# Performance work log

Hardware: AMD Instinct MI355X
Metric: run time of the kernel (lower is better)

The kernel has to match this reference:

```python
import jax, jax.numpy as jnp
import numpy as np


def setup_inputs() -> dict:
    key = jax.random.key(0)
    ks = jax.random.split(key, 4)
    B, S, D, V = 2, 2048, 768, 50257
    scale = 1.0 / np.sqrt(D)
    x = jax.random.normal(ks[0], (B, S, D), dtype=jnp.float32)
    W_vocab = jax.random.normal(ks[1], (V, D), dtype=jnp.float32) * scale
    b_vocab = jnp.zeros((V,), dtype=jnp.float32)
    W_lin = jax.random.normal(ks[2], (D, D), dtype=jnp.float32) * scale
    b_lin = jnp.zeros((D,), dtype=jnp.float32)
    return {"x": x, "W_vocab": W_vocab, "b_vocab": b_vocab, "W_lin": W_lin, "b_lin": b_lin}


def reference(x, W_vocab, b_vocab, W_lin, b_lin):
    # vocab_attention_layer(x): [B,S,D] @ [D,V] + b -> [B,S,V]
    logits = jnp.einsum('bsd,vd->bsv', x, W_vocab) + b_vocab
    va = jax.nn.softmax(logits, axis=-1)                      # [B,S,V]
    # einsum('bij,jk->bik', va, weight): contract vocab against embedding rows
    va_weight = jnp.einsum('bsv,vd->bsd', va, W_vocab)        # [B,S,D]
    # final nn.Linear(d_model, d_model): y = h @ W^T + b
    return jnp.einsum('bsd,ed->bse', va_weight, W_lin) + b_lin
```

## Files before the change

### kernel.cpp

```cpp
#include <hip/hip_runtime.h>
#include <hip/hip_bf16.h>
#include <stdint.h>

typedef float f32x4 __attribute__((ext_vector_type(4)));
typedef short s16x8 __attribute__((ext_vector_type(8)));
typedef unsigned short u16;

#define M_ROWS 4096
#define DIM    768
#define VOCAB  50257
#define VPAD   50304

#define OFF_XB     0ull
#define OFF_WLB    6291456ull
#define OFF_WVB    7471104ull
#define OFF_WVTC   84738048ull
#define OFF_P      100270080ull
#define OFF_ORUN   183107584ull
#define OFF_LROW   195690496ull
#define OFF_BROW   195706880ull
#define OFF_KEYS   195723264ull
#define OFF_H      195723392ull

__device__ __forceinline__ u16 f2bf(float f) {
    union { float f; unsigned u; } x; x.f = f;
    return (u16)((x.u + 0x7fffu + ((x.u >> 16) & 1u)) >> 16);
}
__device__ __forceinline__ float bf2f_hi(unsigned u) {
    union { unsigned u; float f; } x; x.u = u & 0xffff0000u; return x.f;
}
__device__ __forceinline__ float bf2f_lo(unsigned u) {
    union { unsigned u; float f; } x; x.u = u << 16; return x.f;
}
__device__ __forceinline__ unsigned fkey(float f) {
    union { float f; unsigned u; } x; x.f = f;
    return (x.u & 0x80000000u) ? ~x.u : (x.u | 0x80000000u);
}
__device__ __forceinline__ float fkey_dec(unsigned k) {
    union { unsigned u; float f; } x;
    x.u = (k & 0x80000000u) ? (k & 0x7fffffffu) : ~k;
    return x.f;
}
__device__ __forceinline__ void glds16(const u16* g, u16* l) {
    __builtin_amdgcn_global_load_lds(
        (const __attribute__((address_space(1))) unsigned int*)g,
        (__attribute__((address_space(3))) unsigned int*)l,
        16, 0, 0);
}

__global__ __launch_bounds__(256) void cast_bf16(const float* __restrict__ src,
                                                 u16* __restrict__ dst, int n4) {
    int i = blockIdx.x * 256 + threadIdx.x;
    if (i >= n4) return;
    float4 v = ((const float4*)src)[i];
    ushort4 o;
    o.x = f2bf(v.x); o.y = f2bf(v.y); o.z = f2bf(v.z); o.w = f2bf(v.w);
    ((ushort4*)dst)[i] = o;
}

__global__ __launch_bounds__(256) void prep_wvb(const float* __restrict__ wv,
                                                u16* __restrict__ wvb, int ntask) {
    int t = blockIdx.x * 256 + threadIdx.x;
    if (t >= ntask) return;
    int v = t / 96, ch = t % 96;
    uint4 pk = {0u, 0u, 0u, 0u};
    if (v < VOCAB) {
        const float* p = wv + (size_t)v * DIM + ch * 8;
        float4 f0 = ((const float4*)p)[0];
        float4 f1 = ((const float4*)p)[1];
        pk.x = (unsigned)f2bf(f0.x) | ((unsigned)f2bf(f0.y) << 16);
        pk.y = (unsigned)f2bf(f0.z) | ((unsigned)f2bf(f0.w) << 16);
        pk.z = (unsigned)f2bf(f1.x) | ((unsigned)f2bf(f1.y) << 16);
        pk.w = (unsigned)f2bf(f1.z) | ((unsigned)f2bf(f1.w) << 16);
    }
    *(uint4*)(wvb + (size_t)v * DIM + ch * 8) = pk;
}

__global__ void init_keys(unsigned* keys) {
    keys[0] = 0u;
    keys[1] = fkey(-3.0e38f);
}

__global__ __launch_bounds__(256) void wnorm(const u16* __restrict__ wvb,
                                             unsigned* __restrict__ keys) {
    __shared__ float part[128];
    int tid = threadIdx.x;
    int vb = blockIdx.x * 32;
    int vl = tid & 31, cg = tid >> 5;
    float s = 0.f;
    #pragma unroll
    for (int it = 0; it < 12; ++it) {
        int ch = cg + 8 * it;
        uint4 pk = *(const uint4*)(wvb + (size_t)(vb + vl) * DIM + ch * 8);
        const unsigned* pw = (const unsigned*)&pk;
        #pragma unroll
        for (int k = 0; k < 4; ++k) {
            float lo = bf2f_lo(pw[k]), hi = bf2f_hi(pw[k]);
            s += lo * lo + hi * hi;
        }
    }
    s += __shfl_xor(s, 32);
    int w = tid >> 6, lane = tid & 63;
    if (lane < 32) part[w * 32 + lane] = s;
    __syncthreads();
    if (tid < 32) {
        float t = part[tid] + part[32 + tid] + part[64 + tid] + part[96 + tid];
        float n = sqrtf(t);
        #pragma unroll
        for (int msk = 1; msk < 32; msk <<= 1) n = fmaxf(n, __shfl_xor(n, msk));
        if (tid == 0) atomicMax(&keys[0], __float_as_uint(n));
    }
}

__global__ __launch_bounds__(256) void bmax_k(const float* __restrict__ bv,
                                              unsigned* __restrict__ keys) {
    int i = blockIdx.x * 256 + threadIdx.x;
    float v = (i < VOCAB) ? bv[i] : -3.0e38f;
    #pragma unroll
    for (int msk = 1; msk < 64; msk <<= 1) v = fmaxf(v, __shfl_xor(v, msk));
    if ((threadIdx.x & 63) == 0) atomicMax(&keys[1], fkey(v));
}

__global__ __launch_bounds__(256) void xnorm(const float* __restrict__ x,
                                             const unsigned* __restrict__ keys,
                                             float* __restrict__ Brow) {
    int w = threadIdx.x >> 6, lane = threadIdx.x & 63;
    int r = blockIdx.x * 4 + w;
    const float4* p = (const float4*)(x + (size_t)r * DIM);
    float s = 0.f;
    #pragma unroll
    for (int it = 0; it < 3; ++it) {
        float4 v = p[it * 64 + lane];
        s += v.x * v.x + v.y * v.y + v.z * v.z + v.w * v.w;
    }
    #pragma unroll
    for (int msk = 1; msk < 64; msk <<= 1) s += __shfl_xor(s, msk);
    if (lane == 0) {
        float Wn = __uint_as_float(keys[0]);
        float bm = fkey_dec(keys[1]);
        Brow[r] = sqrtf(s) * Wn * 1.01f + bm + 0.1f;
    }
}

__global__ __launch_bounds__(256) void prep_wvt_chunk(const u16* __restrict__ wvb,
                                                      u16* __restrict__ wvtc, int v0) {
    __shared__ u16 tile[32][776];
    int tb = blockIdx.x;
    int tid = threadIdx.x;
    int vb = v0 + tb * 32;
    #pragma unroll
    for (int it = 0; it < 12; ++it) {
        int task = tid + 256 * it;
        int row = task / 96, ch = task % 96;
        uint4 pk = *(const uint4*)(wvb + (size_t)(vb + row) * DIM + ch * 8);
        *(uint4*)(&tile[row][ch * 8]) = pk;
    }
    __syncthreads();
    #pragma unroll
    for (int it = 0; it < 12; ++it) {
        int task = tid + 256 * it;
        int d = task >> 2, vc = task & 3;
        u16 t8[8];
        #pragma unroll
        for (int j = 0; j < 8; ++j) t8[j] = tile[vc * 8 + j][d];
        uint4 pk;
        pk.x = (unsigned)t8[0] | ((unsigned)t8[1] << 16);
        pk.y = (unsigned)t8[2] | ((unsigned)t8[3] << 16);
        pk.z = (unsigned)t8[4] | ((unsigned)t8[5] << 16);
        pk.w = (unsigned)t8[6] | ((unsigned)t8[7] << 16);
        *(uint4*)(wvtc + (size_t)tb * 24576 + d * 32 + vc * 8) = pk;
    }
}

__global__ __launch_bounds__(256, 2) void gemm1(
    const u16* __restrict__ xb, const u16* __restrict__ wvb,
    const float* __restrict__ bvocab, const float* __restrict__ Brow,
    u16* __restrict__ P, float* __restrict__ Lrow, int v0, int pitch) {
    __shared__ u16 SB[17408];
    __shared__ float BL[128];
    u16* At = SB;
    u16* Bt = SB + 4096;
    u16* Ptile = SB;
    int mb = blockIdx.x & 31, nb = blockIdx.x >> 5;
    int tid = threadIdx.x;
    int w = tid >> 6, lane = tid & 63, q = lane >> 4, c = lane & 15;
    int wm = w & 1, wn = w >> 1;
    if (tid < 128) BL[tid] = Brow[mb * 128 + tid];
    int trow = tid >> 2, tch = tid & 3;
    const u16* gA0 = xb + (size_t)(mb * 128 + trow) * DIM + tch * 8;
    const u16* gA1 = xb + (size_t)(mb * 128 + 64 + trow) * DIM + tch * 8;
    const u16* gB0 = wvb + (size_t)(v0 + nb * 128 + trow) * DIM + tch * 8;
    const u16* gB1 = wvb + (size_t)(v0 + nb * 128 + 64 + trow) * DIM + tch * 8;
    f32x4 acc[4][4];
    #pragma unroll
    for (int i = 0; i < 4; ++i)
        #pragma unroll
        for (int j = 0; j < 4; ++j) acc[i][j] = (f32x4){0.f, 0.f, 0.f, 0.f};

    for (int ko = 0; ko < 24; ++ko) {
        glds16(gA0 + ko * 32, At + tid * 8);
        glds16(gA1 + ko * 32, At + (tid + 256) * 8);
        glds16(gB0 + ko * 32, Bt + tid * 8);
        glds16(gB1 + ko * 32, Bt + (tid + 256) * 8);
        __syncthreads();
        s16x8 af[4], bf[4];
        #pragma unroll
        for (int i = 0; i < 4; ++i)
            af[i] = *(const s16x8*)(At + (wm * 64 + i * 16 + c) * 32 + q * 8);
        #pragma unroll
        for (int j = 0; j < 4; ++j)
            bf[j] = *(const s16x8*)(Bt + (wn * 64 + j * 16 + c) * 32 + q * 8);
        #pragma unroll
        for (int i = 0; i < 4; ++i)
            #pragma unroll
            for (int j = 0; j < 4; ++j)
                acc[i][j] = __builtin_amdgcn_mfma_f32_16x16x32_bf16(af[i], bf[j], acc[i][j], 0, 0, 0);
        __syncthreads();
    }
    float bvv[4]; bool vok[4];
    #pragma unroll
    for (int j = 0; j < 4; ++j) {
        int v = v0 + nb * 128 + wn * 64 + j * 16 + c;
        vok[j] = (v < VOCAB);
        bvv[j] = vok[j] ? bvocab[v] : 0.f;
    }
    #pragma unroll
    for (int i = 0; i < 4; ++i) {
        #pragma unroll
        for (int jr = 0; jr < 4; ++jr) {
            int row = wm * 64 + i * 16 + q * 4 + jr;
            float B = BL[row];
            float e[4], sum = 0.f;
            #pragma unroll
            for (int j = 0; j < 4; ++j) {
                float z = acc[i][j][jr] + bvv[j];
                e[j] = vok[j] ? __expf(z - B) : 0.f;
                sum += e[j];
            }
            #pragma unroll
            for (int j = 0; j < 4; ++j)
                Ptile[row * 136 + wn * 64 + j * 16 + c] = f2bf(e[j]);
            sum += __shfl_xor(sum, 1);
            sum += __shfl_xor(sum, 2);
            sum += __shfl_xor(sum, 4);
            sum += __shfl_xor(sum, 8);
            if (c == 0) atomicAdd(&Lrow[mb * 128 + row], sum);
        }
    }
    __syncthreads();
    #pragma unroll
    for (int it = 0; it < 8; ++it) {
        int task = tid + 256 * it;
        int row = task >> 4, ch = task & 15;
        uint4 pk = *(const uint4*)(Ptile + row * 136 + ch * 8);
        *(uint4*)(P + (size_t)(mb * 128 + row) * pitch + nb * 128 + ch * 8) = pk;
    }
}

__global__ __launch_bounds__(256, 2) void gemm2(
    const u16* __restrict__ P, const u16* __restrict__ wvtc,
    float* __restrict__ Orun, int pitch, int kt32_total, int kts) {
    __shared__ u16 At[4096];
    __shared__ u16 Bt[4096];
    int mb = blockIdx.x & 31;
    int rest = blockIdx.x >> 5;
    int nb = rest % 6, s = rest / 6;
    int kt0 = s * kts;
    int kt1 = kt0 + kts; if (kt1 > kt32_total) kt1 = kt32_total;
    int tid = threadIdx.x;
    int w = tid >> 6, lane = tid & 63, q = lane >> 4, c = lane & 15;
    int wm = w & 1, wn = w >> 1;
    int trow = tid >> 2, tch = tid & 3;
    const u16* gA0 = P + (size_t)(mb * 128 + trow) * pitch + tch * 8;
    const u16* gA1 = P + (size_t)(mb * 128 + 64 + trow) * pitch + tch * 8;
    const u16* gB0 = wvtc + (size_t)(nb * 128 + trow) * 32 + tch * 8;
    const u16* gB1 = wvtc + (size_t)(nb * 128 + 64 + trow) * 32 + tch * 8;
    f32x4 acc[4][4];
    #pragma unroll
    for (int i = 0; i < 4; ++i)
        #pragma unroll
        for (int j = 0; j < 4; ++j) acc[i][j] = (f32x4){0.f, 0.f, 0.f, 0.f};

    for (int kt = kt0; kt < kt1; ++kt) {
        glds16(gA0 + kt * 32, At + tid * 8);
        glds16(gA1 + kt * 32, At + (tid + 256) * 8);
        glds16(gB0 + (size_t)kt * 24576, Bt + tid * 8);
        glds16(gB1 + (size_t)kt * 24576, Bt + (tid + 256) * 8);
        __syncthreads();
        s16x8 af[4], bf[4];
        #pragma unroll
        for (int i = 0; i < 4; ++i)
            af[i] = *(const s16x8*)(At + (wm * 64 + i * 16 + c) * 32 + q * 8);
        #pragma unroll
        for (int j = 0; j < 4; ++j)
            bf[j] = *(const s16x8*)(Bt + (wn * 64 + j * 16 + c) * 32 + q * 8);
        #pragma unroll
        for (int i = 0; i < 4; ++i)
            #pragma unroll
            for (int j = 0; j < 4; ++j)
                acc[i][j] = __builtin_amdgcn_mfma_f32_16x16x32_bf16(af[i], bf[j], acc[i][j], 0, 0, 0);
        __syncthreads();
    }
    #pragma unroll
    for (int i = 0; i < 4; ++i)
        #pragma unroll
        for (int j = 0; j < 4; ++j)
            #pragma unroll
            for (int jr = 0; jr < 4; ++jr) {
                int row = mb * 128 + wm * 64 + i * 16 + q * 4 + jr;
                int col = nb * 128 + wn * 64 + j * 16 + c;
                atomicAdd(&Orun[(size_t)row * DIM + col], acc[i][j][jr]);
            }
}

__global__ __launch_bounds__(256) void final_h(const float* __restrict__ Orun,
                                               const float* __restrict__ Lrow,
                                               u16* __restrict__ h) {
    int idx = blockIdx.x * 256 + threadIdx.x;
    if (idx >= M_ROWS * DIM) return;
    int r = idx / DIM;
    h[idx] = f2bf(Orun[idx] / Lrow[r]);
}

__global__ __launch_bounds__(256, 2) void final_gemm(const u16* __restrict__ h,
                                                     const u16* __restrict__ wlb,
                                                     const float* __restrict__ blin,
                                                     float* __restrict__ out) {
    __shared__ u16 At[4096];
    __shared__ u16 Bt[4096];
    int mb = blockIdx.x & 31, eb = blockIdx.x >> 5;
    int tid = threadIdx.x;
    int w = tid >> 6, lane = tid & 63, q = lane >> 4, c = lane & 15;
    int wm = w & 1, wn = w >> 1;
    int trow = tid >> 2, tch = tid & 3;
    const u16* gA0 = h + (size_t)(mb * 128 + trow) * DIM + tch * 8;
    const u16* gA1 = h + (size_t)(mb * 128 + 64 + trow) * DIM + tch * 8;
    const u16* gB0 = wlb + (size_t)(eb * 128 + trow) * DIM + tch * 8;
    const u16* gB1 = wlb + (size_t)(eb * 128 + 64 + trow) * DIM + tch * 8;
    f32x4 acc[4][4];
    #pragma unroll
    for (int i = 0; i < 4; ++i)
        #pragma unroll
        for (int j = 0; j < 4; ++j) acc[i][j] = (f32x4){0.f, 0.f, 0.f, 0.f};

    for (int ko = 0; ko < 24; ++ko) {
        glds16(gA0 + ko * 32, At + tid * 8);
        glds16(gA1 + ko * 32, At + (tid + 256) * 8);
        glds16(gB0 + ko * 32, Bt + tid * 8);
        glds16(gB1 + ko * 32, Bt + (tid + 256) * 8);
        __syncthreads();
        s16x8 af[4], bf[4];
        #pragma unroll
        for (int i = 0; i < 4; ++i)
            af[i] = *(const s16x8*)(At + (wm * 64 + i * 16 + c) * 32 + q * 8);
        #pragma unroll
        for (int j = 0; j < 4; ++j)
            bf[j] = *(const s16x8*)(Bt + (wn * 64 + j * 16 + c) * 32 + q * 8);
        #pragma unroll
        for (int i = 0; i < 4; ++i)
            #pragma unroll
            for (int j = 0; j < 4; ++j)
                acc[i][j] = __builtin_amdgcn_mfma_f32_16x16x32_bf16(af[i], bf[j], acc[i][j], 0, 0, 0);
        __syncthreads();
    }
    #pragma unroll
    for (int j = 0; j < 4; ++j) {
        int e = eb * 128 + wn * 64 + j * 16 + c;
        float bl = blin[e];
        #pragma unroll
        for (int i = 0; i < 4; ++i) {
            #pragma unroll
            for (int jr = 0; jr < 4; ++jr) {
                int row = mb * 128 + wm * 64 + i * 16 + q * 4 + jr;
                out[(size_t)row * DIM + e] = acc[i][j][jr] + bl;
            }
        }
    }
}

extern "C" void kernel_launch(void* const* d_in, const int* in_sizes, int n_in,
                              void* d_out, int out_size, void* d_ws, size_t ws_size,
                              hipStream_t stream) {
    const float* x  = (const float*)d_in[0];
    const float* Wv = (const float*)d_in[1];
    const float* bv = (const float*)d_in[2];
    const float* Wl = (const float*)d_in[3];
    const float* bl = (const float*)d_in[4];
    float* out = (float*)d_out;
    char* ws = (char*)d_ws;

    u16* xb   = (u16*)(ws + OFF_XB);
    u16* wlb  = (u16*)(ws + OFF_WLB);
    u16* wvb  = (u16*)(ws + OFF_WVB);
    u16* wvtc = (u16*)(ws + OFF_WVTC);
    u16* P    = (u16*)(ws + OFF_P);
    float* Orun  = (float*)(ws + OFF_ORUN);
    float* Lrow  = (float*)(ws + OFF_LROW);
    float* Brow  = (float*)(ws + OFF_BROW);
    unsigned* keys = (unsigned*)(ws + OFF_KEYS);
    u16* h       = (u16*)(ws + OFF_H);

    cast_bf16<<<(M_ROWS * DIM / 4 + 255) / 256, 256, 0, stream>>>(x, xb, M_ROWS * DIM / 4);
    cast_bf16<<<(DIM * DIM / 4 + 255) / 256, 256, 0, stream>>>(Wl, wlb, DIM * DIM / 4);
    {
        int ntask = VPAD * 96;
        prep_wvb<<<(ntask + 255) / 256, 256, 0, stream>>>(Wv, wvb, ntask);
    }
    init_keys<<<1, 1, 0, stream>>>(keys);
    hipMemsetAsync(Orun, 0, (size_t)M_ROWS * DIM * 4, stream);
    hipMemsetAsync(Lrow, 0, (size_t)M_ROWS * 4, stream);
    wnorm<<<VPAD / 32, 256, 0, stream>>>(wvb, keys);
    bmax_k<<<(VOCAB + 255) / 256, 256, 0, stream>>>(bv, keys);
    xnorm<<<M_ROWS / 4, 256, 0, stream>>>(x, keys, Brow);

    const int chunk_start[5] = {0, 79, 158, 237, 316};
    const int chunk_nt[5]    = {79, 79, 79, 79, 77};
    for (int cidx = 0; cidx < 5; ++cidx) {
        int nt = chunk_nt[cidx];
        int v0 = chunk_start[cidx] * 128;
        int pitch = nt * 128;
        int kt32 = nt * 4;
        int kts = (kt32 + 3) / 4;
        prep_wvt_chunk<<<nt * 4, 256, 0, stream>>>(wvb, wvtc, v0);
        gemm1<<<nt * 32, 256, 0, stream>>>(xb, wvb, bv, Brow, P, Lrow, v0, pitch);
        gemm2<<<32 * 6 * 4, 256, 0, stream>>>(P, wvtc, Orun, pitch, kt32, kts);
    }
    final_h<<<(M_ROWS * DIM + 255) / 256, 256, 0, stream>>>(Orun, Lrow, h);
    final_gemm<<<192, 256, 0, stream>>>(h, wlb, bl, out);
}
```

Measured before the change: 1.293 ms.

## Use 256x256 double-buffered swizzled MFMA tiles for both vocab GEMMs

Replaces the 128x128, single-buffered, 32-wide-K GEMM loops with a shared 256x256 tile loop that uses 64-wide K, 512 threads, XOR-swizzled LDS, double-buffered global-to-LDS prefetch and barrier/priority phasing around the MFMA groups. The W_vocab transpose moves out of the chunk loop into one full-matrix transpose, and the vocab chunks become 8192 wide (7 chunks) with a split-K gemm2 over 240 blocks. The goal is more operand reuse per byte loaded and better overlap of memory with MFMA work. In exchange it uses 128KB of LDS per block, needs more workspace, keeps fp32 atomics on Orun, and the last chunk is small and may under-fill the GPU.

```diff
diff --git a/kernel.cpp b/kernel.cpp
--- a/kernel.cpp
+++ b/kernel.cpp
@@ -9,18 +9,18 @@
 #define M_ROWS 4096
 #define DIM    768
 #define VOCAB  50257
-#define VPAD   50304
+#define VP2    50432
 
 #define OFF_XB     0ull
 #define OFF_WLB    6291456ull
 #define OFF_WVB    7471104ull
-#define OFF_WVTC   84738048ull
-#define OFF_P      100270080ull
-#define OFF_ORUN   183107584ull
-#define OFF_LROW   195690496ull
-#define OFF_BROW   195706880ull
-#define OFF_KEYS   195723264ull
-#define OFF_H      195723392ull
+#define OFF_WVT    84934656ull
+#define OFF_P      162398208ull
+#define OFF_ORUN   229507072ull
+#define OFF_LROW   242089984ull
+#define OFF_BROW   242106368ull
+#define OFF_KEYS   242122752ull
+#define OFF_H      242122880ull
 
 __device__ __forceinline__ u16 f2bf(float f) {
     union { float f; unsigned u; } x; x.f = f;
@@ -142,175 +142,243 @@
     }
 }
 
-__global__ __launch_bounds__(256) void prep_wvt_chunk(const u16* __restrict__ wvb,
-                                                      u16* __restrict__ wvtc, int v0) {
+__global__ __launch_bounds__(256) void prep_wvt(const u16* __restrict__ wvb,
+                                                u16* __restrict__ wvt) {
     __shared__ u16 tile[32][776];
-    int tb = blockIdx.x;
+    int vb = blockIdx.x * 32;
     int tid = threadIdx.x;
-    int vb = v0 + tb * 32;
     #pragma unroll
     for (int it = 0; it < 12; ++it) {
         int task = tid + 256 * it;
         int row = task / 96, ch = task % 96;
-        uint4 pk = *(const uint4*)(wvb + (size_t)(vb + row) * DIM + ch * 8);
-        *(uint4*)(&tile[row][ch * 8]) = pk;
+        *(uint4*)(&tile[row][ch * 8]) = *(const uint4*)(wvb + (size_t)(vb + row) * DIM + ch * 8);
     }
     __syncthreads();
     #pragma unroll
     for (int it = 0; it < 12; ++it) {
         int task = tid + 256 * it;
-        int d = task >> 2, vc = task & 3;
+        int d = task >> 2, vg = task & 3;
         u16 t8[8];
         #pragma unroll
-        for (int j = 0; j < 8; ++j) t8[j] = tile[vc * 8 + j][d];
+        for (int j = 0; j < 8; ++j) t8[j] = tile[vg * 8 + j][d];
         uint4 pk;
         pk.x = (unsigned)t8[0] | ((unsigned)t8[1] << 16);
         pk.y = (unsigned)t8[2] | ((unsigned)t8[3] << 16);
         pk.z = (unsigned)t8[4] | ((unsigned)t8[5] << 16);
         pk.w = (unsigned)t8[6] | ((unsigned)t8[7] << 16);
-        *(uint4*)(wvtc + (size_t)tb * 24576 + d * 32 + vc * 8) = pk;
-    }
-}
-
-__global__ __launch_bounds__(256, 2) void gemm1(
+        *(uint4*)(wvt + (size_t)d * VP2 + vb + vg * 8) = pk;
+    }
+}
+
+
+template<int MH, int NH>
+__device__ __forceinline__ void mfma_quad(f32x4 (&acc)[8][4],
+                                          const s16x8 (&afr)[4][2],
+                                          const s16x8 (&bfr)[2][2][2]) {
+    #pragma unroll
+    for (int mi = 0; mi < 4; ++mi)
+        #pragma unroll
+        for (int ni = 0; ni < 2; ++ni) {
+            f32x4 a_ = acc[MH * 4 + mi][NH * 2 + ni];
+            a_ = __builtin_amdgcn_mfma_f32_16x16x32_bf16(afr[mi][0], bfr[NH][ni][0], a_, 0, 0, 0);
+            a_ = __builtin_amdgcn_mfma_f32_16x16x32_bf16(afr[mi][1], bfr[NH][ni][1], a_, 0, 0, 0);
+            acc[MH * 4 + mi][NH * 2 + ni] = a_;
+        }
+}
+
+#define STG(g, pitch, rowbase, kcol, ldst) do {                                   \
+    const u16* _s0 = (g) + (size_t)((rowbase) + rlo) * (pitch) + (kcol) + offu;   \
+    const u16* _s1 = _s0 + (size_t)64 * (pitch);                                  \
+    glds16(_s0, (u16*)(ldst) + (size_t)tid * 8);                                  \
+    glds16(_s1, (u16*)(ldst) + (size_t)tid * 8 + 4096);                           \
+} while (0)
+
+#define RD_A(buf, mh) do { _Pragma("unroll")                                              \
+    for (int _mi = 0; _mi < 4; ++_mi) {                                                   \
+        afr[_mi][0] = *(const s16x8*)((buf) + ((abase + ((mh)*4 + _mi)*2048)      ^ asw));\
+        afr[_mi][1] = *(const s16x8*)((buf) + ((abase + ((mh)*4 + _mi)*2048 + 64) ^ asw));\
+    } } while (0)
+
+#define RD_B(buf, nh) do { _Pragma("unroll")                                              \
+    for (int _ni = 0; _ni < 2; ++_ni) {                                                   \
+        bfr[nh][_ni][0] = *(const s16x8*)((buf) + ((bbase + ((nh)*2 + _ni)*2048)      ^ asw));\
+        bfr[nh][_ni][1] = *(const s16x8*)((buf) + ((bbase + ((nh)*2 + _ni)*2048 + 64) ^ asw));\
+    } } while (0)
+
+#define PH_SYNC1() do { __builtin_amdgcn_s_barrier();                      \
+    asm volatile("s_waitcnt lgkmcnt(0)" ::: "memory");                     \
+    __builtin_amdgcn_s_setprio(1); } while (0)
+#define PH_SYNC2() do { __builtin_amdgcn_s_setprio(0);                     \
+    __builtin_amdgcn_s_barrier(); } while (0)
+
+__device__ __forceinline__ void kloop256(char* LDS,
+                                         const u16* __restrict__ gA, int pA,
+                                         const u16* __restrict__ gB, int pB,
+                                         int NT, int tid, f32x4 (&acc)[8][4]) {
+    const int lane = tid & 63, w = tid >> 6;
+    const int c = lane & 15, q = (lane >> 4) & 3;
+    const int wm = w & 1, wn = w >> 1;
+    const int asw = (c & 7) << 4;
+    const int abase = wm * 16384 + c * 128 + q * 16;
+    const int bbase = (wn >> 1) * 16384 + (wn & 1) * 8192 + c * 128 + q * 16;
+    const int rlo = tid >> 3;
+    const int offu = ((tid & 7) * 8) ^ ((rlo & 7) << 3);
+    char* A0 = LDS;
+    char* B0 = LDS + 32768;
+    char* A1 = LDS + 65536;
+    char* B1 = LDS + 98304;
+    s16x8 afr[4][2], bfr[2][2][2];
+    const int ktN = NT - 1;
+
+    STG(gA, pA, 0,   0, A0);
+    STG(gA, pA, 128, 0, A0 + 16384);
+    STG(gB, pB, 0,   0, B0);
+    STG(gB, pB, 128, 0, B0 + 16384);
+    {
+        int k1 = (ktN >= 1 ? 1 : 0) * 64;
+        STG(gB, pB, 0,   k1, B1);
+        STG(gB, pB, 128, k1, B1 + 16384);
+        STG(gA, pA, 0,   k1, A1);
+    }
+    asm volatile("s_waitcnt vmcnt(6)" ::: "memory");
+    __builtin_amdgcn_s_barrier();
+
+    const int nit = NT >> 1;
+    #pragma unroll 1
+    for (int it2 = 0; it2 < nit; ++it2) {
+        int kO  = ((2 * it2 + 1 < NT) ? 2 * it2 + 1 : ktN) * 64;
+        int kN0 = ((2 * it2 + 2 < NT) ? 2 * it2 + 2 : ktN) * 64;
+        int kN1 = ((2 * it2 + 3 < NT) ? 2 * it2 + 3 : ktN) * 64;
+        RD_A(A0, 0); RD_B(B0, 0);
+        STG(gA, pA, 128, kO, A1 + 16384);
+        PH_SYNC1(); mfma_quad<0, 0>(acc, afr, bfr); PH_SYNC2();
+        RD_B(B0, 1);
+        PH_SYNC1(); mfma_quad<0, 1>(acc, afr, bfr); PH_SYNC2();
+        RD_A(A0, 1);
+        STG(gB, pB, 0, kN0, B0);
+        PH_SYNC1(); mfma_quad<1, 0>(acc, afr, bfr); PH_SYNC2();
+        STG(gB, pB, 128, kN0, B0 + 16384);
+        STG(gA, pA, 0,   kN0, A0);
+        asm volatile("s_waitcnt vmcnt(6)" ::: "memory");
+        PH_SYNC1(); mfma_quad<1, 1>(acc, afr, bfr); PH_SYNC2();
+        RD_A(A1, 0); RD_B(B1, 0);
+        STG(gA, pA, 128, kN0, A0 + 16384);
+        PH_SYNC1(); mfma_quad<0, 0>(acc, afr, bfr); PH_SYNC2();
+        RD_B(B1, 1);
+        PH_SYNC1(); mfma_quad<0, 1>(acc, afr, bfr); PH_SYNC2();
+        RD_A(A1, 1);
+        STG(gB, pB, 0, kN1, B1);
+        PH_SYNC1(); mfma_quad<1, 0>(acc, afr, bfr); PH_SYNC2();
+        STG(gB, pB, 128, kN1, B1 + 16384);
+        STG(gA, pA, 0,   kN1, A1);
+        asm volatile("s_waitcnt vmcnt(6)" ::: "memory");
+        PH_SYNC1(); mfma_quad<1, 1>(acc, afr, bfr); PH_SYNC2();
+    }
+}
+
+__global__ __launch_bounds__(512, 2) void gemm1(
     const u16* __restrict__ xb, const u16* __restrict__ wvb,
     const float* __restrict__ bvocab, const float* __restrict__ Brow,
-    u16* __restrict__ P, float* __restrict__ Lrow, int v0, int pitch) {
-    __shared__ u16 SB[17408];
-    __shared__ float BL[128];
-    u16* At = SB;
-    u16* Bt = SB + 4096;
-    u16* Ptile = SB;
-    int mb = blockIdx.x & 31, nb = blockIdx.x >> 5;
+    u16* __restrict__ P, float* __restrict__ Lrow, int v0, int CN) {
+    __shared__ __align__(16) char LDS[131072];
+    __shared__ float BL[256];
     int tid = threadIdx.x;
-    int w = tid >> 6, lane = tid & 63, q = lane >> 4, c = lane & 15;
+    int mt = blockIdx.x & 15, nt = blockIdx.x >> 4;
+    if (tid < 256) BL[tid] = Brow[mt * 256 + tid];
+    f32x4 acc[8][4];
+    #pragma unroll
+    for (int i = 0; i < 8; ++i)
+        #pragma unroll
+        for (int j = 0; j < 4; ++j) acc[i][j] = (f32x4){0.f, 0.f, 0.f, 0.f};
+    kloop256(LDS, xb + (size_t)(mt * 256) * DIM, DIM,
+             wvb + (size_t)(v0 + nt * 256) * DIM, DIM, 12, tid, acc);
+
+    int lane = tid & 63, w = tid >> 6, c = lane & 15, q = (lane >> 4) & 3;
     int wm = w & 1, wn = w >> 1;
-    if (tid < 128) BL[tid] = Brow[mb * 128 + tid];
-    int trow = tid >> 2, tch = tid & 3;
-    const u16* gA0 = xb + (size_t)(mb * 128 + trow) * DIM + tch * 8;
-    const u16* gA1 = xb + (size_t)(mb * 128 + 64 + trow) * DIM + tch * 8;
-    const u16* gB0 = wvb + (size_t)(v0 + nb * 128 + trow) * DIM + tch * 8;
-    const u16* gB1 = wvb + (size_t)(v0 + nb * 128 + 64 + trow) * DIM + tch * 8;
-    f32x4 acc[4][4];
-    #pragma unroll
-    for (int i = 0; i < 4; ++i)
+    float bvv[4]; bool vok[4];
+    #pragma unroll
+    for (int n = 0; n < 4; ++n) {
+        int vg = v0 + nt * 256 + wn * 64 + n * 16 + c;
+        vok[n] = vg < VOCAB;
+        bvv[n] = vok[n] ? bvocab[vg] : 0.f;
+    }
+    #pragma unroll
+    for (int m = 0; m < 8; ++m)
+        #pragma unroll
+        for (int jr = 0; jr < 4; ++jr) {
+            int rloc = wm * 128 + m * 16 + q * 4 + jr;
+            float B = BL[rloc];
+            float s = 0.f;
+            #pragma unroll
+            for (int n = 0; n < 4; ++n) {
+                float z = acc[m][n][jr] + bvv[n];
+                float e = vok[n] ? __expf(z - B) : 0.f;
+                acc[m][n][jr] = e;
+                s += e;
+            }
+            s += __shfl_xor(s, 1); s += __shfl_xor(s, 2);
+            s += __shfl_xor(s, 4); s += __shfl_xor(s, 8);
+            if (c == 0) atomicAdd(&Lrow[mt * 256 + rloc], s);
+        }
+    u16* Pt = (u16*)LDS;
+    #pragma unroll
+    for (int h = 0; h < 2; ++h) {
+        if (h) __syncthreads();
+        if (wm == h) {
+            #pragma unroll
+            for (int m = 0; m < 8; ++m)
+                #pragma unroll
+                for (int jr = 0; jr < 4; ++jr) {
+                    int r = m * 16 + q * 4 + jr;
+                    #pragma unroll
+                    for (int n = 0; n < 4; ++n)
+                        Pt[r * 256 + wn * 64 + n * 16 + c] = f2bf(acc[m][n][jr]);
+                }
+        }
+        __syncthreads();
+        #pragma unroll
+        for (int itc = 0; itc < 8; ++itc) {
+            int task = tid + itc * 512;
+            int r = task >> 5, chn = task & 31;
+            uint4 pk = *(const uint4*)(Pt + r * 256 + chn * 8);
+            *(uint4*)(P + (size_t)(mt * 256 + h * 128 + r) * CN + nt * 256 + chn * 8) = pk;
+        }
+    }
+}
+
+__global__ __launch_bounds__(512, 2) void gemm2(
+    const u16* __restrict__ P, const u16* __restrict__ wvt,
+    float* __restrict__ Orun, int CN, int v0, int KT) {
+    __shared__ __align__(16) char LDS[131072];
+    int tid = threadIdx.x;
+    int mt = blockIdx.x & 15;
+    int rest = blockIdx.x >> 4;
+    int nt = rest % 3, s = rest / 3;
+    int ks0 = ((KT + 9) / 10) * 2;
+    int k0 = s * ks0;
+    if (k0 >= KT) return;
+    int NTs = (k0 + ks0 <= KT) ? ks0 : (KT - k0);
+    f32x4 acc[8][4];
+    #pragma unroll
+    for (int i = 0; i < 8; ++i)
         #pragma unroll
         for (int j = 0; j < 4; ++j) acc[i][j] = (f32x4){0.f, 0.f, 0.f, 0.f};
-
-    for (int ko = 0; ko < 24; ++ko) {
-        glds16(gA0 + ko * 32, At + tid * 8);
-        glds16(gA1 + ko * 32, At + (tid + 256) * 8);
-        glds16(gB0 + ko * 32, Bt + tid * 8);
-        glds16(gB1 + ko * 32, Bt + (tid + 256) * 8);
-        __syncthreads();
-        s16x8 af[4], bf[4];
-        #pragma unroll
-        for (int i = 0; i < 4; ++i)
-            af[i] = *(const s16x8*)(At + (wm * 64 + i * 16 + c) * 32 + q * 8);
-        #pragma unroll
-        for (int j = 0; j < 4; ++j)
-            bf[j] = *(const s16x8*)(Bt + (wn * 64 + j * 16 + c) * 32 + q * 8);
-        #pragma unroll
-        for (int i = 0; i < 4; ++i)
-            #pragma unroll
-            for (int j = 0; j < 4; ++j)
-                acc[i][j] = __builtin_amdgcn_mfma_f32_16x16x32_bf16(af[i], bf[j], acc[i][j], 0, 0, 0);
-        __syncthreads();
-    }
-    float bvv[4]; bool vok[4];
-    #pragma unroll
-    for (int j = 0; j < 4; ++j) {
-        int v = v0 + nb * 128 + wn * 64 + j * 16 + c;
-        vok[j] = (v < VOCAB);
-        bvv[j] = vok[j] ? bvocab[v] : 0.f;
-    }
-    #pragma unroll
-    for (int i = 0; i < 4; ++i) {
-        #pragma unroll
-        for (int jr = 0; jr < 4; ++jr) {
-            int row = wm * 64 + i * 16 + q * 4 + jr;
-            float B = BL[row];
-            float e[4], sum = 0.f;
-            #pragma unroll
-            for (int j = 0; j < 4; ++j) {
-                float z = acc[i][j][jr] + bvv[j];
-                e[j] = vok[j] ? __expf(z - B) : 0.f;
-                sum += e[j];
-            }
-            #pragma unroll
-            for (int j = 0; j < 4; ++j)
-                Ptile[row * 136 + wn * 64 + j * 16 + c] = f2bf(e[j]);
-            sum += __shfl_xor(sum, 1);
-            sum += __shfl_xor(sum, 2);
-            sum += __shfl_xor(sum, 4);
-            sum += __shfl_xor(sum, 8);
-            if (c == 0) atomicAdd(&Lrow[mb * 128 + row], sum);
-        }
-    }
-    __syncthreads();
-    #pragma unroll
-    for (int it = 0; it < 8; ++it) {
-        int task = tid + 256 * it;
-        int row = task >> 4, ch = task & 15;
-        uint4 pk = *(const uint4*)(Ptile + row * 136 + ch * 8);
-        *(uint4*)(P + (size_t)(mb * 128 + row) * pitch + nb * 128 + ch * 8) = pk;
-    }
-}
-
-__global__ __launch_bounds__(256, 2) void gemm2(
-    const u16* __restrict__ P, const u16* __restrict__ wvtc,
-    float* __restrict__ Orun, int pitch, int kt32_total, int kts) {
-    __shared__ u16 At[4096];
-    __shared__ u16 Bt[4096];
-    int mb = blockIdx.x & 31;
-    int rest = blockIdx.x >> 5;
-    int nb = rest % 6, s = rest / 6;
-    int kt0 = s * kts;
-    int kt1 = kt0 + kts; if (kt1 > kt32_total) kt1 = kt32_total;
-    int tid = threadIdx.x;
-    int w = tid >> 6, lane = tid & 63, q = lane >> 4, c = lane & 15;
+    kloop256(LDS, P + (size_t)(mt * 256) * CN + k0 * 64, CN,
+             wvt + (size_t)(nt * 256) * VP2 + v0 + k0 * 64, VP2, NTs, tid, acc);
+
+    int lane = tid & 63, w = tid >> 6, c = lane & 15, q = (lane >> 4) & 3;
     int wm = w & 1, wn = w >> 1;
-    int trow = tid >> 2, tch = tid & 3;
-    const u16* gA0 = P + (size_t)(mb * 128 + trow) * pitch + tch * 8;
-    const u16* gA1 = P + (size_t)(mb * 128 + 64 + trow) * pitch + tch * 8;
-    const u16* gB0 = wvtc + (size_t)(nb * 128 + trow) * 32 + tch * 8;
-    const u16* gB1 = wvtc + (size_t)(nb * 128 + 64 + trow) * 32 + tch * 8;
-    f32x4 acc[4][4];
-    #pragma unroll
-    for (int i = 0; i < 4; ++i)
-        #pragma unroll
-        for (int j = 0; j < 4; ++j) acc[i][j] = (f32x4){0.f, 0.f, 0.f, 0.f};
-
-    for (int kt = kt0; kt < kt1; ++kt) {
-        glds16(gA0 + kt * 32, At + tid * 8);
-        glds16(gA1 + kt * 32, At + (tid + 256) * 8);
-        glds16(gB0 + (size_t)kt * 24576, Bt + tid * 8);
-        glds16(gB1 + (size_t)kt * 24576, Bt + (tid + 256) * 8);
-        __syncthreads();
-        s16x8 af[4], bf[4];
-        #pragma unroll
-        for (int i = 0; i < 4; ++i)
-            af[i] = *(const s16x8*)(At + (wm * 64 + i * 16 + c) * 32 + q * 8);
-        #pragma unroll
-        for (int j = 0; j < 4; ++j)
-            bf[j] = *(const s16x8*)(Bt + (wn * 64 + j * 16 + c) * 32 + q * 8);
-        #pragma unroll
-        for (int i = 0; i < 4; ++i)
-            #pragma unroll
-            for (int j = 0; j < 4; ++j)
-                acc[i][j] = __builtin_amdgcn_mfma_f32_16x16x32_bf16(af[i], bf[j], acc[i][j], 0, 0, 0);
-        __syncthreads();
-    }
-    #pragma unroll
-    for (int i = 0; i < 4; ++i)
-        #pragma unroll
-        for (int j = 0; j < 4; ++j)
+    #pragma unroll
+    for (int m = 0; m < 8; ++m)
+        #pragma unroll
+        for (int n = 0; n < 4; ++n) {
+            int col = nt * 256 + wn * 64 + n * 16 + c;
             #pragma unroll
             for (int jr = 0; jr < 4; ++jr) {
-                int row = mb * 128 + wm * 64 + i * 16 + q * 4 + jr;
-                int col = nb * 128 + wn * 64 + j * 16 + c;
-                atomicAdd(&Orun[(size_t)row * DIM + col], acc[i][j][jr]);
+                int row = mt * 256 + wm * 128 + m * 16 + q * 4 + jr;
+                atomicAdd(&Orun[(size_t)row * DIM + col], acc[m][n][jr]);
             }
+        }
 }
 
 __global__ __launch_bounds__(256) void final_h(const float* __restrict__ Orun,
@@ -392,7 +460,7 @@
     u16* xb   = (u16*)(ws + OFF_XB);
     u16* wlb  = (u16*)(ws + OFF_WLB);
     u16* wvb  = (u16*)(ws + OFF_WVB);
-    u16* wvtc = (u16*)(ws + OFF_WVTC);
+    u16* wvt  = (u16*)(ws + OFF_WVT);
     u16* P    = (u16*)(ws + OFF_P);
     float* Orun  = (float*)(ws + OFF_ORUN);
     float* Lrow  = (float*)(ws + OFF_LROW);
@@ -403,27 +471,26 @@
     cast_bf16<<<(M_ROWS * DIM / 4 + 255) / 256, 256, 0, stream>>>(x, xb, M_ROWS * DIM / 4);
     cast_bf16<<<(DIM * DIM / 4 + 255) / 256, 256, 0, stream>>>(Wl, wlb, DIM * DIM / 4);
     {
-        int ntask = VPAD * 96;
+        int ntask = VP2 * 96;
         prep_wvb<<<(ntask + 255) / 256, 256, 0, stream>>>(Wv, wvb, ntask);
     }
     init_keys<<<1, 1, 0, stream>>>(keys);
     hipMemsetAsync(Orun, 0, (size_t)M_ROWS * DIM * 4, stream);
     hipMemsetAsync(Lrow, 0, (size_t)M_ROWS * 4, stream);
-    wnorm<<<VPAD / 32, 256, 0, stream>>>(wvb, keys);
+    wnorm<<<VP2 / 32, 256, 0, stream>>>(wvb, keys);
     bmax_k<<<(VOCAB + 255) / 256, 256, 0, stream>>>(bv, keys);
     xnorm<<<M_ROWS / 4, 256, 0, stream>>>(x, keys, Brow);
-
-    const int chunk_start[5] = {0, 79, 158, 237, 316};
-    const int chunk_nt[5]    = {79, 79, 79, 79, 77};
-    for (int cidx = 0; cidx < 5; ++cidx) {
-        int nt = chunk_nt[cidx];
-        int v0 = chunk_start[cidx] * 128;
-        int pitch = nt * 128;
-        int kt32 = nt * 4;
-        int kts = (kt32 + 3) / 4;
-        prep_wvt_chunk<<<nt * 4, 256, 0, stream>>>(wvb, wvtc, v0);
-        gemm1<<<nt * 32, 256, 0, stream>>>(xb, wvb, bv, Brow, P, Lrow, v0, pitch);
-        gemm2<<<32 * 6 * 4, 256, 0, stream>>>(P, wvtc, Orun, pitch, kt32, kts);
+    prep_wvt<<<VP2 / 32, 256, 0, stream>>>(wvb, wvt);
+
+    static const int chunk_start[7] = {0, 32, 64, 96, 128, 160, 192};
+    static const int chunk_cnt[7]   = {32, 32, 32, 32, 32, 32, 5};
+    for (int ci = 0; ci < 7; ++ci) {
+        int cnt = chunk_cnt[ci];
+        int v0 = chunk_start[ci] * 256;
+        int CN = cnt * 256;
+        int KT = CN / 64;
+        gemm1<<<16 * cnt, 512, 0, stream>>>(xb, wvb, bv, Brow, P, Lrow, v0, CN);
+        gemm2<<<240, 512, 0, stream>>>(P, wvt, Orun, CN, v0, KT);
     }
     final_h<<<(M_ROWS * DIM + 255) / 256, 256, 0, stream>>>(Orun, Lrow, h);
     final_gemm<<<192, 256, 0, stream>>>(h, wlb, bl, out);
```

Measured after the change: 1.414 ms. 9.3% more time.
